# Kernel tuning notes

Measured on AMD Instinct MI355X. Metric: run time of the kernel, lower is better.

## Reference

```python
import jax, jax.numpy as jnp
import numpy as np

SMOOTH = 4.0      # smoothness_factor
MAX_RATE = 2.0    # maximum_rate
MIN_RATE = 0.0    # minimum_rate
MIN_SHAPE = 1.0   # minimum_shape per dim
INIT_RATE = 1.0   # initial rates value -> determines static output shape


def dct_mat(N):
    """Orthonormal DCT-II matrix: (dct_mat(N) @ x) == dct(x, norm='ortho').

    Mathematically identical to the FFT-based butterfly in the torch source
    with norm='ortho'.
    """
    n = np.arange(N)[None, :]
    k = np.arange(N)[:, None]
    D = np.cos(np.pi * (2 * n + 1) * k / (2 * N)) * np.sqrt(2.0 / N)
    D[0] *= 1.0 / np.sqrt(2.0)
    return jnp.asarray(D, dtype=jnp.float32)


def span_mask(threshold, softness, pos):
    # adaptive-span ramp mask (Sukhbaatar et al. 2019), clamped to [0, 1]
    return jnp.clip((softness + threshold - pos) / softness, 0.0, 1.0)


def setup_inputs() -> dict:
    key = jax.random.key(0)
    x = jax.random.normal(key, (32, 64, 128, 128), dtype=jnp.float32)
    rate_weights = jnp.ones((2,), dtype=jnp.float32)  # nn.Parameter init = rates
    return {"x": x, "rate_weights": rate_weights}


def reference(x, rate_weights):
    B, C, H, W = x.shape
    cur = jnp.array([H, W], dtype=jnp.float32)

    # rate clamping (maximum_shape is None -> constrain_max_shape stays False)
    min_allowed = jnp.maximum((jnp.array([MIN_SHAPE, MIN_SHAPE]) - SMOOTH) / cur,
                              jnp.array([MIN_RATE, MIN_RATE]))
    max_allowed = jnp.array([MAX_RATE, MAX_RATE], dtype=jnp.float32)
    r = jnp.clip(rate_weights, min_allowed, max_allowed)

    new_smooth = cur * r + SMOOTH  # traced float, drives the soft mask
    # static output shape from the initial rate values (jit-compatible;
    # matches torch's int(new_shape_smooth) + 1 for the init rates)
    new_h = int(H * INIT_RATE + SMOOTH) + 1  # H + 5
    new_w = int(W * INIT_RATE + SMOOTH) + 1  # W + 5

    # 2D orthonormal DCT-II over the last two dims
    Dh, Dw = dct_mat(H), dct_mat(W)
    freq = jnp.einsum('ui,bcij,vj->bcuv', Dh, x, Dw)  # [B,C,H,W]

    # zero-pad high frequencies up to the new (larger) shape
    freq = jnp.pad(freq, ((0, 0), (0, 0),
                          (0, max(new_h - H, 0)), (0, max(new_w - W, 0))))

    # adaptive-span masks over frequency positions
    vpos = jnp.arange(new_h, dtype=jnp.float32)
    hpos = jnp.arange(new_w, dtype=jnp.float32)
    crop = new_smooth - SMOOTH  # = cur * r
    vmask = span_mask(crop[0], SMOOTH, vpos)  # [new_h]
    hmask = span_mask(crop[1], SMOOTH, hpos)  # [new_w]
    freq = freq * vmask[None, None, :, None] * hmask[None, None, None, :]

    # 2D orthonormal inverse DCT (DCT-III) at the new resolution
    Dh2, Dw2 = dct_mat(new_h), dct_mat(new_w)
    out = jnp.einsum('ui,bcuv,vj->bcij', Dh2, freq, Dw2)  # [B,C,new_h,new_w]
    return out
```

## Files before the change

kernel.cpp:

```cpp
#include <hip/hip_runtime.h>
#include <hip/hip_bf16.h>
#include <math.h>

#define NSLICE 2048
#define NH 133
#define NP 144
#define NT 576

#define M1B  32768
#define SCR  69632
#define LDSB 78848

typedef __attribute__((ext_vector_type(8))) short bf16x8;
typedef __attribute__((ext_vector_type(4))) float f32x4;

typedef __attribute__((address_space(3))) unsigned int  lds_u32;
typedef const __attribute__((address_space(1))) unsigned int glb_u32;

#define GLOAD_LDS16(gsrc, ldst) \
    __builtin_amdgcn_global_load_lds((glb_u32*)(gsrc), (lds_u32*)(ldst), 16, 0, 0)

__device__ __forceinline__ unsigned f2bf(float f) {
    __hip_bfloat16 h = __float2bfloat16(f);
    union { __hip_bfloat16 b; unsigned short u; } c; c.b = h; return (unsigned)c.u;
}

__global__ void prep_M(const float* __restrict__ rw,
                       unsigned short* __restrict__ M1,
                       unsigned short* __restrict__ M2) {
    __shared__ float t1[512];
    __shared__ float t2[532];
    const int b   = blockIdx.x;
    const int m   = b / NP;
    const int row = b - m * NP;
    const int p   = threadIdx.x;

    const float c1  = (float)(M_PI / 256.0);
    const float c2  = (float)(M_PI / 266.0);
    const float s1n = 0.125f;
    const float s10 = 0.08838834764831844f;
    const float s2n = 0.12262786485246718f;
    const float s20 = 0.08671099951921386f;

    for (int k = p; k < 512; k += 128) t1[k] = cosf((float)k * c1) * s1n;
    for (int k = p; k < 532; k += 128) t2[k] = cosf((float)k * c2) * s2n;
    __syncthreads();

    float val = 0.0f;
    if (row < NH) {
        float r = rw[m];
        float minr = fmaxf((1.0f - 4.0f) / 128.0f, 0.0f);
        r = fminf(fmaxf(r, minr), 2.0f);
        const float crop = 128.0f * r;

        const int tp = 2 * p + 1;
        const int ti = 2 * row + 1;
        float acc = s10 * s20;
        int a1 = 0, a2 = 0;
        for (int u = 1; u < 128; ++u) {
            a1 = (a1 + tp) & 511;
            a2 += ti; if (a2 >= 532) a2 -= 532;
            float mask = fminf(fmaxf((4.0f + crop - (float)u) * 0.25f, 0.0f), 1.0f);
            acc = fmaf(t1[a1] * mask, t2[a2], acc);
        }
        val = acc;
    }
    const unsigned short v16 = (unsigned short)f2bf(val);
    if (m == 0) {
        const int it = row >> 4, rr = row & 15;
        const int k2 = p >> 5, gg = (p >> 3) & 3, e = p & 7;
        M1[(size_t)((it * 4 + k2) * 512 + (gg * 16 + rr) * 8 + e)] = v16;
    } else {
        M2[(size_t)row * 128 + p] = v16;
    }
}

__global__ __launch_bounds__(NT, 5) void dct_resize(
        const float* __restrict__ x,
        const unsigned short* __restrict__ M1f,
        const unsigned short* __restrict__ M2,
        float* __restrict__ out) {
    __shared__ __align__(16) unsigned char lds[LDSB];

    const int tid  = threadIdx.x;
    const int w    = tid >> 6;
    const int lane = tid & 63;
    const int r    = lane & 15;
    const int g    = lane >> 4;

    const float* xs = x + (size_t)blockIdx.x * (128 * 128);
    float*       os = out + (size_t)blockIdx.x * (NH * NH);

    const int j0 = w * 16;

    f32x4 xlo[4], xhi[4];
    if (w < 8) {
        #pragma unroll
        for (int v = 0; v < 4; ++v) {
            const int f  = v * 8 + w;
            const int pt = f >> 2, k2 = f & 3;
            const float* src = xs + (size_t)(pt * 16 + r) * 128 + k2 * 32 + g * 8;
            asm volatile("global_load_dwordx4 %0, %1, off"
                         : "=v"(xlo[v]) : "v"(src) : "memory");
            asm volatile("global_load_dwordx4 %0, %1, off offset:16"
                         : "=v"(xhi[v]) : "v"(src) : "memory");
        }
    }

    #pragma unroll
    for (int v = 0; v < 4; ++v)
        GLOAD_LDS16(M1f + (size_t)(v * NT + tid) * 8,
                    lds + M1B + (v * NT + tid) * 16);

    bf16x8 bm2[4];
    #pragma unroll
    for (int kk = 0; kk < 4; ++kk)
        bm2[kk] = *(const bf16x8*)(M2 + (size_t)(j0 + r) * 128 + kk * 32 + g * 8);

    asm volatile("s_waitcnt vmcnt(0)" ::: "memory");
    __builtin_amdgcn_sched_barrier(0);

    if (w < 8) {
        #pragma unroll
        for (int v = 0; v < 4; ++v) {
            const int f = v * 8 + w;
            uint4 pkt;
            pkt.x = f2bf(xlo[v].x) | (f2bf(xlo[v].y) << 16);
            pkt.y = f2bf(xlo[v].z) | (f2bf(xlo[v].w) << 16);
            pkt.z = f2bf(xhi[v].x) | (f2bf(xhi[v].y) << 16);
            pkt.w = f2bf(xhi[v].z) | (f2bf(xhi[v].w) << 16);
            *(uint4*)(lds + f * 1024 + lane * 16) = pkt;
        }
    }
    __syncthreads();

    uint2 u2[8];
    #pragma unroll
    for (int pt = 0; pt < 8; ++pt) {
        f32x4 acc = {0.f, 0.f, 0.f, 0.f};
        #pragma unroll
        for (int kk = 0; kk < 4; ++kk) {
            bf16x8 a = *(const bf16x8*)(lds + (pt * 4 + kk) * 1024 + lane * 16);
            acc = __builtin_amdgcn_mfma_f32_16x16x32_bf16(a, bm2[kk], acc, 0, 0, 0);
        }
        u2[pt].x = f2bf(acc[0]) | (f2bf(acc[1]) << 16);
        u2[pt].y = f2bf(acc[2]) | (f2bf(acc[3]) << 16);
    }

    unsigned char* scr = lds + SCR + w * 1024;
    bf16x8 bfrag[4];
    #pragma unroll
    for (int kk = 0; kk < 4; ++kk) {
        *(uint2*)(scr + (g)     * 128 + r * 8) = u2[2 * kk];
        *(uint2*)(scr + (4 + g) * 128 + r * 8) = u2[2 * kk + 1];
        const uint2 lo2 = *(const uint2*)(scr + (2 * g)     * 128 + r * 8);
        const uint2 hi2 = *(const uint2*)(scr + (2 * g + 1) * 128 + r * 8);
        union { uint4 u; bf16x8 b; } cv;
        cv.u = make_uint4(lo2.x, lo2.y, hi2.x, hi2.y);
        bfrag[kk] = cv.b;
    }

    const int jc = j0 + r;
    #pragma unroll
    for (int it = 0; it < 9; ++it) {
        f32x4 acc = {0.f, 0.f, 0.f, 0.f};
        #pragma unroll
        for (int kk = 0; kk < 4; ++kk) {
            bf16x8 a = *(const bf16x8*)(lds + M1B + (it * 4 + kk) * 1024 + lane * 16);
            acc = __builtin_amdgcn_mfma_f32_16x16x32_bf16(a, bfrag[kk], acc, 0, 0, 0);
        }
        if (jc < NH) {
            #pragma unroll
            for (int q = 0; q < 4; ++q) {
                const int i = it * 16 + g * 4 + q;
                if (i < NH) os[(size_t)i * NH + jc] = acc[q];
            }
        }
    }
}

extern "C" void kernel_launch(void* const* d_in, const int* in_sizes, int n_in,
                              void* d_out, int out_size, void* d_ws, size_t ws_size,
                              hipStream_t stream) {
    const float* x  = (const float*)d_in[0];
    const float* rw = (const float*)d_in[1];
    float* outp = (float*)d_out;
    unsigned short* M1 = (unsigned short*)d_ws;
    unsigned short* M2 = M1 + 18432;

    prep_M<<<dim3(2 * NP), dim3(128), 0, stream>>>(rw, M1, M2);
    dct_resize<<<dim3(NSLICE), dim3(NT), 0, stream>>>(x, M1, M2, outp);
}
```

Baseline: 81.97 us.

## Process four slices per block with register prefetch of next slice input

Each block now handles four consecutive slices instead of one, so the M1 matrix load into LDS and the M2 fragment loads are amortized across slices. The next slice's input is prefetched into registers during the current slice's first GEMM, then converted and written to LDS after a barrier. This aims to hide global load latency and cut per-block setup, at the cost of fewer blocks (512 vs 2048), extra barriers, and higher register pressure that may hurt occupancy or leave CUs idle.

```diff
diff --git a/kernel.cpp b/kernel.cpp
--- a/kernel.cpp
+++ b/kernel.cpp
@@ -4,8 +4,11 @@
 
 #define NSLICE 2048
 #define NH 133
+#define NHH (NH * NH)
 #define NP 144
 #define NT 576
+#define SPB 4
+#define NBLK (NSLICE / SPB)
 
 #define M1B  32768
 #define SCR  69632
@@ -88,24 +91,19 @@
     const int r    = lane & 15;
     const int g    = lane >> 4;
 
-    const float* xs = x + (size_t)blockIdx.x * (128 * 128);
-    float*       os = out + (size_t)blockIdx.x * (NH * NH);
+    const float* xbase = x   + (size_t)blockIdx.x * SPB * (128 * 128);
+    float*       obase = out + (size_t)blockIdx.x * SPB * NHH;
 
     const int j0 = w * 16;
 
-    f32x4 xlo[4], xhi[4];
-    if (w < 8) {
-        #pragma unroll
-        for (int v = 0; v < 4; ++v) {
-            const int f  = v * 8 + w;
-            const int pt = f >> 2, k2 = f & 3;
-            const float* src = xs + (size_t)(pt * 16 + r) * 128 + k2 * 32 + g * 8;
-            asm volatile("global_load_dwordx4 %0, %1, off"
-                         : "=v"(xlo[v]) : "v"(src) : "memory");
-            asm volatile("global_load_dwordx4 %0, %1, off offset:16"
-                         : "=v"(xhi[v]) : "v"(src) : "memory");
-        }
-    }
+    #define SRCOFF(v) ((size_t)(((((v) * 8 + w) >> 2) * 16 + r) * 128 \
+                       + (((v) * 8 + w) & 3) * 32 + g * 8))
+
+    #define ALOAD(dstlo, dsthi, sp) do {                                       \
+        asm volatile("global_load_dwordx4 %0, %1, off"                         \
+                     : "=v"(dstlo) : "v"(sp) : "memory");                      \
+        asm volatile("global_load_dwordx4 %0, %1, off offset:16"               \
+                     : "=v"(dsthi) : "v"(sp) : "memory"); } while (0)
 
     #pragma unroll
     for (int v = 0; v < 4; ++v)
@@ -117,6 +115,11 @@
     for (int kk = 0; kk < 4; ++kk)
         bm2[kk] = *(const bf16x8*)(M2 + (size_t)(j0 + r) * 128 + kk * 32 + g * 8);
 
+    f32x4 xlo[4], xhi[4];
+    if (w < 8) {
+        #pragma unroll
+        for (int v = 0; v < 4; ++v) ALOAD(xlo[v], xhi[v], xbase + SRCOFF(v));
+    }
     asm volatile("s_waitcnt vmcnt(0)" ::: "memory");
     __builtin_amdgcn_sched_barrier(0);
 
@@ -134,49 +137,88 @@
     }
     __syncthreads();
 
-    uint2 u2[8];
-    #pragma unroll
-    for (int pt = 0; pt < 8; ++pt) {
-        f32x4 acc = {0.f, 0.f, 0.f, 0.f};
+    for (int s = 0; s < SPB; ++s) {
+        const bool pf = (s + 1 < SPB);
+
+        if (pf && w < 8) {
+            const float* nx = xbase + (size_t)(s + 1) * (128 * 128);
+            ALOAD(xlo[0], xhi[0], nx + SRCOFF(0));
+            ALOAD(xlo[1], xhi[1], nx + SRCOFF(1));
+        }
+
+        uint2 u2[8];
+        #pragma unroll
+        for (int pt = 0; pt < 8; ++pt) {
+            if (pt == 4 && pf && w < 8) {
+                const float* nx = xbase + (size_t)(s + 1) * (128 * 128);
+                ALOAD(xlo[2], xhi[2], nx + SRCOFF(2));
+                ALOAD(xlo[3], xhi[3], nx + SRCOFF(3));
+            }
+            f32x4 acc = {0.f, 0.f, 0.f, 0.f};
+            #pragma unroll
+            for (int kk = 0; kk < 4; ++kk) {
+                bf16x8 a = *(const bf16x8*)(lds + (pt * 4 + kk) * 1024 + lane * 16);
+                acc = __builtin_amdgcn_mfma_f32_16x16x32_bf16(a, bm2[kk], acc, 0, 0, 0);
+            }
+            u2[pt].x = f2bf(acc[0]) | (f2bf(acc[1]) << 16);
+            u2[pt].y = f2bf(acc[2]) | (f2bf(acc[3]) << 16);
+        }
+
+        unsigned char* scr = lds + SCR + w * 1024;
+        bf16x8 bfrag[4];
         #pragma unroll
         for (int kk = 0; kk < 4; ++kk) {
-            bf16x8 a = *(const bf16x8*)(lds + (pt * 4 + kk) * 1024 + lane * 16);
-            acc = __builtin_amdgcn_mfma_f32_16x16x32_bf16(a, bm2[kk], acc, 0, 0, 0);
-        }
-        u2[pt].x = f2bf(acc[0]) | (f2bf(acc[1]) << 16);
-        u2[pt].y = f2bf(acc[2]) | (f2bf(acc[3]) << 16);
-    }
-
-    unsigned char* scr = lds + SCR + w * 1024;
-    bf16x8 bfrag[4];
-    #pragma unroll
-    for (int kk = 0; kk < 4; ++kk) {
-        *(uint2*)(scr + (g)     * 128 + r * 8) = u2[2 * kk];
-        *(uint2*)(scr + (4 + g) * 128 + r * 8) = u2[2 * kk + 1];
-        const uint2 lo2 = *(const uint2*)(scr + (2 * g)     * 128 + r * 8);
-        const uint2 hi2 = *(const uint2*)(scr + (2 * g + 1) * 128 + r * 8);
-        union { uint4 u; bf16x8 b; } cv;
-        cv.u = make_uint4(lo2.x, lo2.y, hi2.x, hi2.y);
-        bfrag[kk] = cv.b;
-    }
-
-    const int jc = j0 + r;
-    #pragma unroll
-    for (int it = 0; it < 9; ++it) {
-        f32x4 acc = {0.f, 0.f, 0.f, 0.f};
-        #pragma unroll
-        for (int kk = 0; kk < 4; ++kk) {
-            bf16x8 a = *(const bf16x8*)(lds + M1B + (it * 4 + kk) * 1024 + lane * 16);
-            acc = __builtin_amdgcn_mfma_f32_16x16x32_bf16(a, bfrag[kk], acc, 0, 0, 0);
-        }
-        if (jc < NH) {
+            *(uint2*)(scr + (g)     * 128 + r * 8) = u2[2 * kk];
+            *(uint2*)(scr + (4 + g) * 128 + r * 8) = u2[2 * kk + 1];
+            const uint2 lo2 = *(const uint2*)(scr + (2 * g)     * 128 + r * 8);
+            const uint2 hi2 = *(const uint2*)(scr + (2 * g + 1) * 128 + r * 8);
+            union { uint4 u; bf16x8 b; } cv;
+            cv.u = make_uint4(lo2.x, lo2.y, hi2.x, hi2.y);
+            bfrag[kk] = cv.b;
+        }
+
+        __syncthreads();
+
+        if (pf) {
+            asm volatile("s_waitcnt vmcnt(0)" ::: "memory");
+            __builtin_amdgcn_sched_barrier(0);
+            if (w < 8) {
+                #pragma unroll
+                for (int v = 0; v < 4; ++v) {
+                    const int f = v * 8 + w;
+                    uint4 pkt;
+                    pkt.x = f2bf(xlo[v].x) | (f2bf(xlo[v].y) << 16);
+                    pkt.y = f2bf(xlo[v].z) | (f2bf(xlo[v].w) << 16);
+                    pkt.z = f2bf(xhi[v].x) | (f2bf(xhi[v].y) << 16);
+                    pkt.w = f2bf(xhi[v].z) | (f2bf(xhi[v].w) << 16);
+                    *(uint4*)(lds + f * 1024 + lane * 16) = pkt;
+                }
+            }
+        }
+
+        float* os = obase + (size_t)s * NHH;
+        const int jc = j0 + r;
+        #pragma unroll
+        for (int it = 0; it < 9; ++it) {
+            f32x4 acc = {0.f, 0.f, 0.f, 0.f};
             #pragma unroll
-            for (int q = 0; q < 4; ++q) {
-                const int i = it * 16 + g * 4 + q;
-                if (i < NH) os[(size_t)i * NH + jc] = acc[q];
-            }
-        }
-    }
+            for (int kk = 0; kk < 4; ++kk) {
+                bf16x8 a = *(const bf16x8*)(lds + M1B + (it * 4 + kk) * 1024 + lane * 16);
+                acc = __builtin_amdgcn_mfma_f32_16x16x32_bf16(a, bfrag[kk], acc, 0, 0, 0);
+            }
+            if (jc < NH) {
+                #pragma unroll
+                for (int q = 0; q < 4; ++q) {
+                    const int i = it * 16 + g * 4 + q;
+                    if (i < NH) os[(size_t)i * NH + jc] = acc[q];
+                }
+            }
+        }
+
+        __syncthreads();
+    }
+    #undef SRCOFF
+    #undef ALOAD
 }
 
 extern "C" void kernel_launch(void* const* d_in, const int* in_sizes, int n_in,
@@ -189,5 +231,5 @@
     unsigned short* M2 = M1 + 18432;
 
     prep_M<<<dim3(2 * NP), dim3(128), 0, stream>>>(rw, M1, M2);
-    dct_resize<<<dim3(NSLICE), dim3(NT), 0, stream>>>(x, M1, M2, outp);
-}
+    dct_resize<<<dim3(NBLK), dim3(NT), 0, stream>>>(x, M1, M2, outp);
+}
```

Result: slower. 158.8 us (+93.7%).
